# Optimization experiments

Hardware: AMD Instinct MI355X
Metric: run time of the kernel (lower is better)

## Reference

```python
import jax, jax.numpy as jnp
import numpy as np

N = 100000          # nodes
C = 25000           # clusters in coding tree
E = 1000000         # edges
D = 64              # num_features == hidden_dim
NUM_BLOCKS = 2
N_CONVS = 2 * NUM_BLOCKS + 1
BN_EPS = 1e-5


def setup_inputs() -> dict:
    key = jax.random.key(0)
    ks = jax.random.split(key, 8)
    sc = 1.0 / np.sqrt(D)
    x = jax.random.normal(ks[0], (N, D), jnp.float32)
    edge_index = jax.random.randint(ks[1], (2, E), 0, N, dtype=jnp.int32)
    s_cluster = jax.random.randint(ks[2], (N,), 0, C, dtype=jnp.int32)
    conv_w = jax.random.normal(ks[3], (N_CONVS, D, D), jnp.float32) * sc
    conv_b = jnp.zeros((N_CONVS, D), jnp.float32)
    pool_w = jax.random.normal(ks[4], (2, D, D), jnp.float32) * sc
    pool_b = jnp.zeros((2, D), jnp.float32)
    bn_gamma = jnp.ones((2, D), jnp.float32)
    bn_beta = jnp.zeros((2, D), jnp.float32)
    return {"x": x, "edge_index": edge_index, "s_cluster": s_cluster,
            "conv_w": conv_w, "conv_b": conv_b, "pool_w": pool_w,
            "pool_b": pool_b, "bn_gamma": bn_gamma, "bn_beta": bn_beta}


def _gcn_norm(edge_index):
    # GCNConv default: add self-loops, symmetric normalization D^-1/2 (A+I) D^-1/2
    loop = jnp.arange(N, dtype=edge_index.dtype)
    row = jnp.concatenate([edge_index[0], loop])  # source nodes
    col = jnp.concatenate([edge_index[1], loop])  # target nodes
    deg = jax.ops.segment_sum(jnp.ones(row.shape[0], jnp.float32), col, num_segments=N)
    dinv = jnp.where(deg > 0, jax.lax.rsqrt(deg), 0.0)
    return row, col, dinv[row] * dinv[col]  # per-edge norm coefficient


def _gcn_conv(x, w, b, row, col, norm):
    h = x @ w                                     # [N, D] transform first (PyG GCNConv)
    msg = h[row] * norm[:, None]                  # gather + scale, [E+N, D]
    return jax.ops.segment_sum(msg, col, num_segments=N) + b


def _sepool(x, src_idx, dst_idx, out_size, w, b, gamma, beta):
    # SEPooling: scatter-add aggregation then nn = Linear -> ReLU -> BatchNorm1d
    agg = jax.ops.segment_sum(x[src_idx], dst_idx, num_segments=out_size)
    h = jax.nn.relu(agg @ w + b)
    mean = jnp.mean(h, axis=0)
    var = jnp.mean((h - mean) ** 2, axis=0)       # biased var, torch BN training mode
    return gamma * (h - mean) * jax.lax.rsqrt(var + BN_EPS) + beta


def reference(x, edge_index, s_cluster, conv_w, conv_b, pool_w, pool_b, bn_gamma, bn_beta):
    row, col, norm = _gcn_norm(edge_index)
    node_ids = jnp.arange(N, dtype=s_cluster.dtype)
    for i in range(NUM_BLOCKS):
        x = jax.nn.relu(_gcn_conv(x, conv_w[i], conv_b[i], row, col, norm))
    # pool down: nodes -> clusters (s_edge_index = [cluster, node], target_to_source)
    x = jax.nn.relu(_sepool(x, node_ids, s_cluster, C,
                            pool_w[0], pool_b[0], bn_gamma[0], bn_beta[0]))
    # pool up: clusters -> nodes (transposed assignment)
    x = jax.nn.relu(_sepool(x, s_cluster, node_ids, N,
                            pool_w[1], pool_b[1], bn_gamma[1], bn_beta[1]))
    for i in range(NUM_BLOCKS, 2 * NUM_BLOCKS):
        x = jax.nn.relu(_gcn_conv(x, conv_w[i], conv_b[i], row, col, norm))
    x = _gcn_conv(x, conv_w[N_CONVS - 1], conv_b[N_CONVS - 1], row, col, norm)
    return x
```

## Files before the change

### kernel.cpp

```cpp
#include <hip/hip_runtime.h>
#include <hip/hip_bf16.h>

#define NN 100000
#define CC 25000
#define EE 1000000
#define BN_EPS 1e-5f
#define NBINS 1563
#define BINCAP 1024
#define CHUNK 8192
#define SRCMASK 0x03FFFFFFu

typedef unsigned int u32;
typedef unsigned short u16;

__device__ __forceinline__ float lo2f(u32 p) { return __uint_as_float(p << 16); }
__device__ __forceinline__ float hi2f(u32 p) { return __uint_as_float(p & 0xFFFF0000u); }
__device__ __forceinline__ u16 f2bf(float f) {
    u32 u = __float_as_uint(f);
    u32 r = u + 0x7FFFu + ((u >> 16) & 1u);
    return (u16)(r >> 16);
}
__device__ __forceinline__ u32 pack2(float a, float b) {
    return (u32)f2bf(a) | ((u32)f2bf(b) << 16);
}

__global__ void init_misc_kernel(int* __restrict__ bincur, int* __restrict__ cdeg,
                                 float* __restrict__ stats) {
    int i = blockIdx.x * blockDim.x + threadIdx.x;
    if (i < NBINS) bincur[i] = i * BINCAP;
    if (i < CC) cdeg[i] = 0;
    if (i < 256) stats[i] = 0.f;
}

__global__ void hist_kernel(const int* __restrict__ idx, int* __restrict__ deg, int n) {
    int e = blockIdx.x * blockDim.x + threadIdx.x;
    if (e < n) atomicAdd(&deg[idx[e]], 1);
}

__global__ __launch_bounds__(256) void bin_scatter_kernel(
    const int* __restrict__ row, const int* __restrict__ col,
    int* __restrict__ bincur, u32* __restrict__ edges, int E)
{
    __shared__ int cnt[NBINS];
    __shared__ int basep[NBINS];
    const int tid = threadIdx.x;
    const int e0 = blockIdx.x * CHUNK;
    const int e1 = min(e0 + CHUNK, E);
    for (int i = tid; i < NBINS; i += 256) cnt[i] = 0;
    __syncthreads();

    for (int i = e0 + tid; i < e1; i += 1024) {
        const int i1 = i + 256, i2 = i + 512, i3 = i + 768;
        int c0 = col[i];
        int c1 = (i1 < e1) ? col[i1] : 0;
        int c2 = (i2 < e1) ? col[i2] : 0;
        int c3 = (i3 < e1) ? col[i3] : 0;
        atomicAdd(&cnt[c0 >> 6], 1);
        if (i1 < e1) atomicAdd(&cnt[c1 >> 6], 1);
        if (i2 < e1) atomicAdd(&cnt[c2 >> 6], 1);
        if (i3 < e1) atomicAdd(&cnt[c3 >> 6], 1);
    }
    __syncthreads();

    for (int i = tid; i < NBINS; i += 256) {
        int c = cnt[i];
        if (c) basep[i] = atomicAdd(&bincur[i], c);
        cnt[i] = 0;
    }
    __syncthreads();

    for (int i = e0 + tid; i < e1; i += 1024) {
        const int i1 = i + 256, i2 = i + 512, i3 = i + 768;
        int c0 = col[i],                 r0 = row[i];
        int c1 = (i1 < e1) ? col[i1] : 0, r1 = (i1 < e1) ? row[i1] : 0;
        int c2 = (i2 < e1) ? col[i2] : 0, r2 = (i2 < e1) ? row[i2] : 0;
        int c3 = (i3 < e1) ? col[i3] : 0, r3 = (i3 < e1) ? row[i3] : 0;
        {
            int b = c0 >> 6;
            int p = basep[b] + atomicAdd(&cnt[b], 1);
            if (p < (b + 1) * BINCAP) edges[p] = (u32)r0 | ((u32)(c0 & 63) << 26);
        }
        if (i1 < e1) {
            int b = c1 >> 6;
            int p = basep[b] + atomicAdd(&cnt[b], 1);
            if (p < (b + 1) * BINCAP) edges[p] = (u32)r1 | ((u32)(c1 & 63) << 26);
        }
        if (i2 < e1) {
            int b = c2 >> 6;
            int p = basep[b] + atomicAdd(&cnt[b], 1);
            if (p < (b + 1) * BINCAP) edges[p] = (u32)r2 | ((u32)(c2 & 63) << 26);
        }
        if (i3 < e1) {
            int b = c3 >> 6;
            int p = basep[b] + atomicAdd(&cnt[b], 1);
            if (p < (b + 1) * BINCAP) edges[p] = (u32)r3 | ((u32)(c3 & 63) << 26);
        }
    }
}

__global__ __launch_bounds__(256) void deg_dinv_kernel(
    const int* __restrict__ bincur, const u32* __restrict__ edges,
    int* __restrict__ deg, float* __restrict__ dinv, int M)
{
    __shared__ int cnt[64];
    const int tid = threadIdx.x;
    if (tid < 64) cnt[tid] = 0;
    __syncthreads();
    const int eb = blockIdx.x * BINCAP;
    const int ee = min(bincur[blockIdx.x], eb + BINCAP);
    for (int i = eb + tid; i < ee; i += 256)
        atomicAdd(&cnt[edges[i] >> 26], 1);
    __syncthreads();
    const int node = blockIdx.x * 64 + tid;
    if (tid < 64 && node < M) {
        deg[node] = cnt[tid];
        dinv[node] = rsqrtf((float)(cnt[tid] + 1));
    }
}

__global__ __launch_bounds__(256) void csr_scatter_kernel(
    const int* __restrict__ bincur, const u32* __restrict__ edges,
    const int* __restrict__ rowptr, int* __restrict__ csrc, int M)
{
    __shared__ int cur[64];
    const int tid = threadIdx.x;
    const int base = blockIdx.x * 64;
    if (tid < 64) cur[tid] = (base + tid < M) ? rowptr[base + tid] : 0;
    __syncthreads();
    const int eb = blockIdx.x * BINCAP;
    const int ee = min(bincur[blockIdx.x], eb + BINCAP);
    for (int i = eb + tid; i < ee; i += 256) {
        u32 pk = edges[i];
        int slot = atomicAdd(&cur[pk >> 26], 1);
        csrc[slot] = (int)(pk & SRCMASK);
    }
}

__global__ __launch_bounds__(256) void scan_block_kernel(const int* __restrict__ in,
                                                         int* __restrict__ out,
                                                         int* __restrict__ bsum, int n) {
    __shared__ int sh[256];
    const int tid = threadIdx.x;
    const int base = blockIdx.x * 1024 + tid * 4;
    int v0 = 0, v1 = 0, v2 = 0, v3 = 0;
    if (base + 0 < n) v0 = in[base + 0];
    if (base + 1 < n) v1 = in[base + 1];
    if (base + 2 < n) v2 = in[base + 2];
    if (base + 3 < n) v3 = in[base + 3];
    int s = v0 + v1 + v2 + v3;
    sh[tid] = s;
    __syncthreads();
    for (int off = 1; off < 256; off <<= 1) {
        int t = (tid >= off) ? sh[tid - off] : 0;
        __syncthreads();
        sh[tid] += t;
        __syncthreads();
    }
    int excl = sh[tid] - s;
    if (tid == 255) bsum[blockIdx.x] = sh[255];
    if (base + 0 < n) out[base + 0] = excl;
    if (base + 1 < n) out[base + 1] = excl + v0;
    if (base + 2 < n) out[base + 2] = excl + v0 + v1;
    if (base + 3 < n) out[base + 3] = excl + v0 + v1 + v2;
}

__global__ __launch_bounds__(256) void scan_top_kernel(int* __restrict__ bsum, int nb) {
    __shared__ int sh[256];
    const int tid = threadIdx.x;
    int v = (tid < nb) ? bsum[tid] : 0;
    sh[tid] = v;
    __syncthreads();
    for (int off = 1; off < 256; off <<= 1) {
        int t = (tid >= off) ? sh[tid - off] : 0;
        __syncthreads();
        sh[tid] += t;
        __syncthreads();
    }
    if (tid < nb) bsum[tid] = sh[tid] - v;
}

__global__ __launch_bounds__(256) void scan_add_kernel(int* __restrict__ p, int* __restrict__ cursor,
                                                       const int* __restrict__ bsum, int n, int total) {
    const int base = blockIdx.x * 1024;
    const int off = bsum[blockIdx.x];
    for (int j = threadIdx.x; j < 1024; j += 256) {
        int i = base + j;
        if (i < n) { int v = p[i] + off; p[i] = v; cursor[i] = v; }
    }
    if (blockIdx.x == 0 && threadIdx.x == 0) p[n] = total;
}

__global__ void scatter_iota_kernel(const int* __restrict__ cl,
                                    int* __restrict__ cursor, int* __restrict__ dst, int n) {
    int i = blockIdx.x * blockDim.x + threadIdx.x;
    if (i < n) { int p = atomicAdd(&cursor[cl[i]], 1); dst[p] = i; }
}

template <bool INF32, bool EDGEDINV, bool AFFINE>
__device__ __forceinline__ void acc_row(const void* __restrict__ Pv,
                                        const float* __restrict__ dinv, int r, int lc,
                                        const float* av, const float* bv,
                                        float& s0, float& s1, float& s2, float& s3) {
    float d = EDGEDINV ? dinv[r] : 1.0f;
    float v0, v1, v2, v3;
    if constexpr (INF32) {
        float4 v = ((const float4*)Pv)[(size_t)r * 16 + lc];
        v0 = v.x; v1 = v.y; v2 = v.z; v3 = v.w;
    } else {
        uint2 p = ((const uint2*)Pv)[(size_t)r * 16 + lc];
        v0 = lo2f(p.x); v1 = hi2f(p.x); v2 = lo2f(p.y); v3 = hi2f(p.y);
    }
    if constexpr (AFFINE) {
        v0 = fmaxf(fmaf(av[0], v0, bv[0]), 0.f);
        v1 = fmaxf(fmaf(av[1], v1, bv[1]), 0.f);
        v2 = fmaxf(fmaf(av[2], v2, bv[2]), 0.f);
        v3 = fmaxf(fmaf(av[3], v3, bv[3]), 0.f);
    }
    if constexpr (EDGEDINV) {
        s0 = fmaf(v0, d, s0); s1 = fmaf(v1, d, s1);
        s2 = fmaf(v2, d, s2); s3 = fmaf(v3, d, s3);
    } else { s0 += v0; s1 += v1; s2 += v2; s3 += v3; }
}

template <int MODE, bool INF32, bool AFFINE, bool SCALEOUT, bool RELU, bool OUTF32>
__global__ __launch_bounds__(256, 8) void fused_mm_kernel(
    const int* __restrict__ rowptr, const int* __restrict__ src,
    const void* __restrict__ Pv, const float* __restrict__ W,
    const float* __restrict__ bias, const float* __restrict__ dinv,
    const float* __restrict__ bst, const float* __restrict__ bng,
    const float* __restrict__ bnb, float invM,
    void* __restrict__ out, int M)
{
    __shared__ float Xs[64 * 68];

    const int tid = threadIdx.x;
    const int base = blockIdx.x * 64;

    {
        const int g = tid >> 4;
        const int lc = tid & 15;

        float av[4] = {0.f, 0.f, 0.f, 0.f};
        float bvv[4] = {0.f, 0.f, 0.f, 0.f};
        if constexpr (AFFINE) {
            #pragma unroll
            for (int j = 0; j < 4; j++) {
                int c = lc * 4 + j;
                float m = bst[c] * invM;
                float var = bst[64 + c] * invM - m * m;
                float rs = rsqrtf(var + BN_EPS);
                av[j] = bng[c] * rs;
                bvv[j] = bnb[c] - m * av[j];
            }
        }

        #pragma unroll
        for (int q = 0; q < 4; q++) {
            const int nl = g * 4 + q;
            const int node = base + nl;
            float s0 = 0.f, s1 = 0.f, s2 = 0.f, s3 = 0.f;
            if (node < M) {
                if constexpr (MODE == 2) {
                    acc_row<INF32, false, AFFINE>(Pv, dinv, src[node], lc, av, bvv, s0, s1, s2, s3);
                } else {
                    if constexpr (MODE == 0)
                        acc_row<INF32, true, AFFINE>(Pv, dinv, node, lc, av, bvv, s0, s1, s2, s3);
                    int i = rowptr[node];
                    const int pe = rowptr[node + 1];
                    for (; i + 4 <= pe; i += 4) {
                        int r0 = src[i], r1 = src[i + 1], r2 = src[i + 2], r3 = src[i + 3];
                        acc_row<INF32, MODE == 0, AFFINE>(Pv, dinv, r0, lc, av, bvv, s0, s1, s2, s3);
                        acc_row<INF32, MODE == 0, AFFINE>(Pv, dinv, r1, lc, av, bvv, s0, s1, s2, s3);
                        acc_row<INF32, MODE == 0, AFFINE>(Pv, dinv, r2, lc, av, bvv, s0, s1, s2, s3);
                        acc_row<INF32, MODE == 0, AFFINE>(Pv, dinv, r3, lc, av, bvv, s0, s1, s2, s3);
                    }
                    for (; i < pe; i++)
                        acc_row<INF32, MODE == 0, AFFINE>(Pv, dinv, src[i], lc, av, bvv, s0, s1, s2, s3);
                }
            }
            *(float4*)&Xs[nl * 68 + lc * 4] = make_float4(s0, s1, s2, s3);
        }
    }
    __syncthreads();

    const int c4 = tid & 15;
    const int rg = tid >> 4;
    const float* Wc = W + c4 * 4;

    float acc[4][4];
    #pragma unroll
    for (int r = 0; r < 4; r++)
        #pragma unroll
        for (int c = 0; c < 4; c++) acc[r][c] = 0.f;

    #pragma unroll 4
    for (int k0 = 0; k0 < 64; k0 += 4) {
        float4 w0 = *(const float4*)&Wc[(k0 + 0) * 64];
        float4 w1 = *(const float4*)&Wc[(k0 + 1) * 64];
        float4 w2 = *(const float4*)&Wc[(k0 + 2) * 64];
        float4 w3 = *(const float4*)&Wc[(k0 + 3) * 64];
        #pragma unroll
        for (int r = 0; r < 4; r++) {
            float4 xv = *(const float4*)&Xs[(rg * 4 + r) * 68 + k0];
            acc[r][0] = fmaf(xv.x, w0.x, acc[r][0]);
            acc[r][1] = fmaf(xv.x, w0.y, acc[r][1]);
            acc[r][2] = fmaf(xv.x, w0.z, acc[r][2]);
            acc[r][3] = fmaf(xv.x, w0.w, acc[r][3]);
            acc[r][0] = fmaf(xv.y, w1.x, acc[r][0]);
            acc[r][1] = fmaf(xv.y, w1.y, acc[r][1]);
            acc[r][2] = fmaf(xv.y, w1.z, acc[r][2]);
            acc[r][3] = fmaf(xv.y, w1.w, acc[r][3]);
            acc[r][0] = fmaf(xv.z, w2.x, acc[r][0]);
            acc[r][1] = fmaf(xv.z, w2.y, acc[r][1]);
            acc[r][2] = fmaf(xv.z, w2.z, acc[r][2]);
            acc[r][3] = fmaf(xv.z, w2.w, acc[r][3]);
            acc[r][0] = fmaf(xv.w, w3.x, acc[r][0]);
            acc[r][1] = fmaf(xv.w, w3.y, acc[r][1]);
            acc[r][2] = fmaf(xv.w, w3.z, acc[r][2]);
            acc[r][3] = fmaf(xv.w, w3.w, acc[r][3]);
        }
    }

    const float4 bv = *(const float4*)&bias[c4 * 4];
    #pragma unroll
    for (int r = 0; r < 4; r++) {
        int gr = base + rg * 4 + r;
        if (gr < M) {
            float v0 = acc[r][0], v1 = acc[r][1], v2 = acc[r][2], v3 = acc[r][3];
            if constexpr (SCALEOUT) {
                float d = dinv[gr];
                v0 *= d; v1 *= d; v2 *= d; v3 *= d;
            }
            v0 += bv.x; v1 += bv.y; v2 += bv.z; v3 += bv.w;
            if constexpr (RELU) {
                v0 = fmaxf(v0, 0.f); v1 = fmaxf(v1, 0.f);
                v2 = fmaxf(v2, 0.f); v3 = fmaxf(v3, 0.f);
            }
            if constexpr (OUTF32)
                ((float4*)out)[(size_t)gr * 16 + c4] = make_float4(v0, v1, v2, v3);
            else
                ((uint2*)out)[(size_t)gr * 16 + c4] = make_uint2(pack2(v0, v1), pack2(v2, v3));
        }
    }
}

__global__ __launch_bounds__(256) void bn_stats_kernel(const u32* __restrict__ H,
                                                       float* __restrict__ stats, int M)
{
    const int tid = threadIdx.x;
    const int c2 = tid & 31;
    const int rg = tid >> 5;
    float a0 = 0.f, a1 = 0.f, b0 = 0.f, b1 = 0.f;
    for (int r = blockIdx.x * 8 + rg; r < M; r += gridDim.x * 8) {
        u32 p = H[(size_t)r * 32 + c2];
        float x0 = lo2f(p), x1 = hi2f(p);
        a0 += x0; a1 += x1; b0 += x0 * x0; b1 += x1 * x1;
    }
    __shared__ float s0[256], s1[256], q0[256], q1[256];
    s0[tid] = a0; s1[tid] = a1; q0[tid] = b0; q1[tid] = b1;
    __syncthreads();
    if (tid < 64) {
        int cc2 = tid >> 1, sub = tid & 1;
        const float* sa = sub ? s1 : s0;
        const float* qa = sub ? q1 : q0;
        float a = 0.f, b = 0.f;
        #pragma unroll
        for (int g8 = 0; g8 < 8; g8++) { a += sa[g8 * 32 + cc2]; b += qa[g8 * 32 + cc2]; }
        atomicAdd(&stats[tid], a);
        atomicAdd(&stats[64 + tid], b);
    }
}

extern "C" void kernel_launch(void* const* d_in, const int* in_sizes, int n_in,
                              void* d_out, int out_size, void* d_ws, size_t ws_size,
                              hipStream_t stream)
{
    const float* x     = (const float*)d_in[0];
    const int*   ei    = (const int*)  d_in[1];
    const int*   scl   = (const int*)  d_in[2];
    const float* cw    = (const float*)d_in[3];
    const float* cb    = (const float*)d_in[4];
    const float* pw    = (const float*)d_in[5];
    const float* pb    = (const float*)d_in[6];
    const float* gamma = (const float*)d_in[7];
    const float* beta  = (const float*)d_in[8];
    float* out = (float*)d_out;

    const int N = NN, C = CC, E = EE;
    const int* row = ei;
    const int* col = ei + E;

    char* w = (char*)d_ws;
    u16* A        = (u16*)w;              w += (size_t)N * 64 * 2;
    u16* B        = (u16*)w;              w += (size_t)N * 64 * 2;
    u16* cb1      = (u16*)w;              w += (size_t)C * 64 * 2;
    float* dinv   = (float*)w;            w += (size_t)N * 4;
    float* stats  = (float*)w;            w += 256 * 4;
    int* deg_i    = (int*)w;              w += (size_t)N * 4;
    int* rowptr   = (int*)w;              w += (size_t)(N + 4) * 4;
    int* cursor   = (int*)w;              w += (size_t)N * 4;
    int* csrc     = (int*)w;              w += (size_t)E * 4;
    u32* edges    = (u32*)w;              w += (size_t)NBINS * BINCAP * 4;
    int* bincur   = (int*)w;              w += (size_t)NBINS * 4;
    int* cdeg     = (int*)w;              w += (size_t)C * 4;
    int* crowptr  = (int*)w;              w += (size_t)(C + 4) * 4;
    int* ccursor  = (int*)w;              w += (size_t)C * 4;
    int* cnsrc    = (int*)w;              w += (size_t)N * 4;
    int* bsum     = (int*)w;              w += 256 * 4;

    float* stats0 = stats;
    float* stats1 = stats + 128;

    const int TB = 256;
    dim3 blk(TB);
    const int NB_N = (N + 1023) / 1024;
    const int NB_C = (C + 1023) / 1024;
    const int NCHUNK = (E + CHUNK - 1) / CHUNK;
    const int GN = NBINS;
    const int GC = (C + 63) / 64;

    init_misc_kernel<<<(C + TB - 1) / TB, blk, 0, stream>>>(bincur, cdeg, stats);
    bin_scatter_kernel<<<NCHUNK, blk, 0, stream>>>(row, col, bincur, edges, E);
    deg_dinv_kernel<<<NBINS, blk, 0, stream>>>(bincur, edges, deg_i, dinv, N);

    scan_block_kernel<<<NB_N, blk, 0, stream>>>(deg_i, rowptr, bsum, N);
    scan_top_kernel<<<1, blk, 0, stream>>>(bsum, NB_N);
    scan_add_kernel<<<NB_N, blk, 0, stream>>>(rowptr, cursor, bsum, N, E);
    csr_scatter_kernel<<<NBINS, blk, 0, stream>>>(bincur, edges, rowptr, csrc, N);

    hist_kernel<<<(N + TB - 1) / TB, blk, 0, stream>>>(scl, cdeg, N);
    scan_block_kernel<<<NB_C, blk, 0, stream>>>(cdeg, crowptr, bsum, C);
    scan_top_kernel<<<1, blk, 0, stream>>>(bsum, NB_C);
    scan_add_kernel<<<NB_C, blk, 0, stream>>>(crowptr, ccursor, bsum, C, N);
    scatter_iota_kernel<<<(N + TB - 1) / TB, blk, 0, stream>>>(scl, ccursor, cnsrc, N);

    fused_mm_kernel<0, true, false, true, true, false>
        <<<GN, blk, 0, stream>>>(rowptr, csrc, x, cw + 0 * 4096, cb + 0 * 64, dinv,
                                 nullptr, nullptr, nullptr, 0.f, A, N);
    fused_mm_kernel<0, false, false, true, true, false>
        <<<GN, blk, 0, stream>>>(rowptr, csrc, A, cw + 1 * 4096, cb + 1 * 64, dinv,
                                 nullptr, nullptr, nullptr, 0.f, B, N);

    fused_mm_kernel<1, false, false, false, true, false>
        <<<GC, blk, 0, stream>>>(crowptr, cnsrc, B, pw, pb, nullptr,
                                 nullptr, nullptr, nullptr, 0.f, cb1, C);
    bn_stats_kernel<<<512, blk, 0, stream>>>((const u32*)cb1, stats0, C);

    fused_mm_kernel<2, false, true, false, true, false>
        <<<GN, blk, 0, stream>>>(nullptr, scl, cb1, pw + 4096, pb + 64, nullptr,
                                 stats0, gamma, beta, 1.0f / C, A, N);
    bn_stats_kernel<<<512, blk, 0, stream>>>((const u32*)A, stats1, N);

    fused_mm_kernel<0, false, true, true, true, false>
        <<<GN, blk, 0, stream>>>(rowptr, csrc, A, cw + 2 * 4096, cb + 2 * 64, dinv,
                                 stats1, gamma + 64, beta + 64, 1.0f / N, B, N);
    fused_mm_kernel<0, false, false, true, true, false>
        <<<GN, blk, 0, stream>>>(rowptr, csrc, B, cw + 3 * 4096, cb + 3 * 64, dinv,
                                 nullptr, nullptr, nullptr, 0.f, A, N);
    fused_mm_kernel<0, false, false, true, false, true>
        <<<GN, blk, 0, stream>>>(rowptr, csrc, A, cw + 4 * 4096, cb + 4 * 64, dinv,
                                 nullptr, nullptr, nullptr, 0.f, out, N);
}
```

Before: 368.8 us.

## Sort edges by source slice and gather GCN neighbors in slice-synchronized passes

Adds a per-bin counting sort that orders each destination bin's edges by source-node slice (8192 nodes per slice). The MODE 0 gather then walks the slices in lockstep across the block, with a barrier after each slice, so that concurrently running blocks tend to touch the same window of source rows and get more L2 reuse. This costs an extra sort pass over the edges, 13 block barriers per conv tile, and branchier per-node loops that may lose memory-level parallelism.

```diff
diff --git a/kernel.cpp b/kernel.cpp
--- a/kernel.cpp
+++ b/kernel.cpp
@@ -8,6 +8,8 @@
 #define NBINS 1563
 #define BINCAP 1024
 #define CHUNK 8192
+#define SLICE_SHIFT 13
+#define NSLICES 13
 #define SRCMASK 0x03FFFFFFu
 
 typedef unsigned int u32;
@@ -95,6 +97,35 @@
             int p = basep[b] + atomicAdd(&cnt[b], 1);
             if (p < (b + 1) * BINCAP) edges[p] = (u32)r3 | ((u32)(c3 & 63) << 26);
         }
+    }
+}
+
+__global__ __launch_bounds__(256) void bin_sort_kernel(
+    const int* __restrict__ bincur, u32* __restrict__ edges)
+{
+    __shared__ u32 buf[BINCAP];
+    __shared__ int cnt[16];
+    __shared__ int off[16];
+    const int tid = threadIdx.x;
+    const int eb = blockIdx.x * BINCAP;
+    const int ee = min(bincur[blockIdx.x], eb + BINCAP);
+    const int n = ee - eb;
+    for (int i = tid; i < n; i += 256) buf[i] = edges[eb + i];
+    if (tid < 16) cnt[tid] = 0;
+    __syncthreads();
+    for (int i = tid; i < n; i += 256)
+        atomicAdd(&cnt[(buf[i] & SRCMASK) >> SLICE_SHIFT], 1);
+    __syncthreads();
+    if (tid == 0) {
+        int s = 0;
+        #pragma unroll
+        for (int k = 0; k < 16; k++) { off[k] = s; s += cnt[k]; }
+    }
+    __syncthreads();
+    for (int i = tid; i < n; i += 256) {
+        u32 e = buf[i];
+        int p = atomicAdd(&off[(e & SRCMASK) >> SLICE_SHIFT], 1);
+        edges[eb + p] = e;
     }
 }
 
@@ -254,34 +285,75 @@
             }
         }
 
-        #pragma unroll
-        for (int q = 0; q < 4; q++) {
-            const int nl = g * 4 + q;
-            const int node = base + nl;
-            float s0 = 0.f, s1 = 0.f, s2 = 0.f, s3 = 0.f;
-            if (node < M) {
-                if constexpr (MODE == 2) {
-                    acc_row<INF32, false, AFFINE>(Pv, dinv, src[node], lc, av, bvv, s0, s1, s2, s3);
-                } else {
-                    if constexpr (MODE == 0)
-                        acc_row<INF32, true, AFFINE>(Pv, dinv, node, lc, av, bvv, s0, s1, s2, s3);
-                    int i = rowptr[node];
-                    const int pe = rowptr[node + 1];
-                    for (; i + 4 <= pe; i += 4) {
-                        int r0 = src[i], r1 = src[i + 1], r2 = src[i + 2], r3 = src[i + 3];
-                        acc_row<INF32, MODE == 0, AFFINE>(Pv, dinv, r0, lc, av, bvv, s0, s1, s2, s3);
-                        acc_row<INF32, MODE == 0, AFFINE>(Pv, dinv, r1, lc, av, bvv, s0, s1, s2, s3);
-                        acc_row<INF32, MODE == 0, AFFINE>(Pv, dinv, r2, lc, av, bvv, s0, s1, s2, s3);
-                        acc_row<INF32, MODE == 0, AFFINE>(Pv, dinv, r3, lc, av, bvv, s0, s1, s2, s3);
+        if constexpr (MODE == 0) {
+            int cur[4], end[4];
+            #pragma unroll
+            for (int q = 0; q < 4; q++) {
+                const int nl = g * 4 + q;
+                const int node = base + nl;
+                float s0 = 0.f, s1 = 0.f, s2 = 0.f, s3 = 0.f;
+                if (node < M) {
+                    cur[q] = rowptr[node];
+                    end[q] = rowptr[node + 1];
+                    acc_row<INF32, true, AFFINE>(Pv, dinv, node, lc, av, bvv, s0, s1, s2, s3);
+                } else { cur[q] = 0; end[q] = 0; }
+                *(float4*)&Xs[nl * 68 + lc * 4] = make_float4(s0, s1, s2, s3);
+            }
+            for (int s = 0; s < NSLICES; s++) {
+                #pragma unroll
+                for (int q = 0; q < 4; q++) {
+                    int i = cur[q];
+                    const int e = end[q];
+                    if (i < e) {
+                        int r = src[i];
+                        if ((r >> SLICE_SHIFT) <= s) {
+                            const int nl = g * 4 + q;
+                            float s0 = 0.f, s1 = 0.f, s2 = 0.f, s3 = 0.f;
+                            do {
+                                acc_row<INF32, true, AFFINE>(Pv, dinv, r, lc, av, bvv,
+                                                             s0, s1, s2, s3);
+                                if (++i >= e) break;
+                                r = src[i];
+                            } while ((r >> SLICE_SHIFT) <= s);
+                            cur[q] = i;
+                            float4 xv = *(float4*)&Xs[nl * 68 + lc * 4];
+                            xv.x += s0; xv.y += s1; xv.z += s2; xv.w += s3;
+                            *(float4*)&Xs[nl * 68 + lc * 4] = xv;
+                        }
                     }
-                    for (; i < pe; i++)
-                        acc_row<INF32, MODE == 0, AFFINE>(Pv, dinv, src[i], lc, av, bvv, s0, s1, s2, s3);
                 }
+                __syncthreads();
             }
-            *(float4*)&Xs[nl * 68 + lc * 4] = make_float4(s0, s1, s2, s3);
-        }
-    }
-    __syncthreads();
+        } else {
+            #pragma unroll
+            for (int q = 0; q < 4; q++) {
+                const int nl = g * 4 + q;
+                const int node = base + nl;
+                float s0 = 0.f, s1 = 0.f, s2 = 0.f, s3 = 0.f;
+                if (node < M) {
+                    if constexpr (MODE == 2) {
+                        acc_row<INF32, false, AFFINE>(Pv, dinv, src[node], lc, av, bvv,
+                                                      s0, s1, s2, s3);
+                    } else {
+                        int i = rowptr[node];
+                        const int pe = rowptr[node + 1];
+                        for (; i + 4 <= pe; i += 4) {
+                            int r0 = src[i], r1 = src[i + 1], r2 = src[i + 2], r3 = src[i + 3];
+                            acc_row<INF32, false, AFFINE>(Pv, dinv, r0, lc, av, bvv, s0, s1, s2, s3);
+                            acc_row<INF32, false, AFFINE>(Pv, dinv, r1, lc, av, bvv, s0, s1, s2, s3);
+                            acc_row<INF32, false, AFFINE>(Pv, dinv, r2, lc, av, bvv, s0, s1, s2, s3);
+                            acc_row<INF32, false, AFFINE>(Pv, dinv, r3, lc, av, bvv, s0, s1, s2, s3);
+                        }
+                        for (; i < pe; i++)
+                            acc_row<INF32, false, AFFINE>(Pv, dinv, src[i], lc, av, bvv,
+                                                          s0, s1, s2, s3);
+                    }
+                }
+                *(float4*)&Xs[nl * 68 + lc * 4] = make_float4(s0, s1, s2, s3);
+            }
+            __syncthreads();
+        }
+    }
 
     const int c4 = tid & 15;
     const int rg = tid >> 4;
@@ -421,6 +493,7 @@
 
     init_misc_kernel<<<(C + TB - 1) / TB, blk, 0, stream>>>(bincur, cdeg, stats);
     bin_scatter_kernel<<<NCHUNK, blk, 0, stream>>>(row, col, bincur, edges, E);
+    bin_sort_kernel<<<NBINS, blk, 0, stream>>>(bincur, edges);
     deg_dinv_kernel<<<NBINS, blk, 0, stream>>>(bincur, edges, deg_i, dinv, N);
 
     scan_block_kernel<<<NB_N, blk, 0, stream>>>(deg_i, rowptr, bsum, N);
```

After: 742.3 us. +101.3%, slower.
